# Kernel optimization log

Hardware: AMD Instinct MI355X
Metric: run time of the kernel (lower is better)

The kernel has to match this reference:

```python
import jax, jax.numpy as jnp
import numpy as np

EMBEDDING_DIM = 100
M = 50                      # chunk width
NUM_CHUNK = EMBEDDING_DIM // M  # 2
VOCAB = 100000
EPS = 1e-8                  # torch CosineSimilarity eps


def setup_inputs() -> dict:
    key = jax.random.key(0)
    k_idx, k_emb, k_w, k_u = jax.random.split(key, 4)
    word_idxs = jax.random.randint(k_idx, (4096, 200), 0, VOCAB)  # [B, L]
    # embedding table initialized uniform(-1, 1) as in the original np.random.uniform
    emb_table = jax.random.uniform(k_emb, (VOCAB, EMBEDDING_DIM), dtype=jnp.float32,
                                   minval=-1.0, maxval=1.0)
    weights = jnp.ones((EMBEDDING_DIM, 1), dtype=jnp.float32)      # output projection
    attend_u = jnp.ones((NUM_CHUNK, M), dtype=jnp.float32)         # per-chunk attention query
    return {"word_idxs": word_idxs, "emb_table": emb_table,
            "weights": weights, "attend_u": attend_u}


def reference(word_idxs, emb_table, weights, attend_u):
    B, L = word_idxs.shape
    embeds = emb_table[word_idxs]                       # [B, L, 100]
    ch = embeds.reshape(B, L, NUM_CHUNK, M)             # [B, L, C, M]
    # cosine similarity per word vs per-chunk query (torch eps semantics)
    e_norm = ch / jnp.maximum(jnp.linalg.norm(ch, axis=-1, keepdims=True), EPS)
    u_norm = attend_u / jnp.maximum(jnp.linalg.norm(attend_u, axis=-1, keepdims=True), EPS)
    cos = jnp.einsum('blcm,cm->blc', e_norm, u_norm)    # [B, L, C]
    alphas = jnp.exp(cos)                               # positive -> L1 norm == sum
    norm_alphas = alphas / jnp.sum(alphas, axis=1, keepdims=True)
    hidden = jnp.einsum('blcm,blc->bcm', ch, norm_alphas).reshape(B, EMBEDDING_DIM)
    return hidden @ weights                             # [B, 1]
```

## Files before the change

kernel.cpp:

```cpp
#include <hip/hip_runtime.h>

constexpr int C_ = 2;
constexpr int M_ = 50;
constexpr int ED = 100;
constexpr float EPS = 1e-8f;

constexpr int ROWS = 128;
constexpr int PAD  = 101;

__global__ __launch_bounds__(128) void row_stats_kernel(
    const float* __restrict__ emb,
    const float* __restrict__ wgt,
    const float* __restrict__ att,
    float4*      __restrict__ tbl,
    int vocab)
{
    __shared__ float  s_rows[ROWS * PAD];
    __shared__ float2 s_uw[ED];
    __shared__ float  s_su[C_];

    const int t  = threadIdx.x;
    const int r0 = blockIdx.x * ROWS;

    if (t < ED) s_uw[t] = make_float2(att[t], wgt[t]);
    __syncthreads();
    if (t < C_) {
        float ss = 0.f;
        #pragma unroll
        for (int m = 0; m < M_; ++m) { float v = s_uw[t * M_ + m].x; ss += v * v; }
        s_su[t] = 1.0f / fmaxf(sqrtf(ss), EPS);
    }

    const int nrows = min(ROWS, vocab - r0);
    const int nvec  = nrows * (ED / 4);
    const float4* src = reinterpret_cast<const float4*>(emb + (long long)r0 * ED);
    for (int i = t; i < nvec; i += 128) {
        const float4 v = src[i];
        const int F   = i * 4;
        const int row = F / ED;
        const int col = F - row * ED;
        float* d = &s_rows[row * PAD + col];
        d[0] = v.x; d[1] = v.y; d[2] = v.z; d[3] = v.w;
    }
    __syncthreads();

    if (t < nrows) {
        const float* row = &s_rows[t * PAD];
        float sq0 = 0.f, sq1 = 0.f, du0 = 0.f, du1 = 0.f, dw0 = 0.f, dw1 = 0.f;
        #pragma unroll
        for (int e = 0; e < M_; ++e) {
            const float x = row[e];
            const float2 uw = s_uw[e];
            sq0 += x * x; du0 = fmaf(x, uw.x, du0); dw0 = fmaf(x, uw.y, dw0);
        }
        #pragma unroll
        for (int e = M_; e < ED; ++e) {
            const float x = row[e];
            const float2 uw = s_uw[e];
            sq1 += x * x; du1 = fmaf(x, uw.x, du1); dw1 = fmaf(x, uw.y, dw1);
        }
        const float c0 = du0 / fmaxf(sqrtf(sq0), EPS) * s_su[0];
        const float c1 = du1 / fmaxf(sqrtf(sq1), EPS) * s_su[1];
        const float a0 = __expf(c0);
        const float a1 = __expf(c1);
        tbl[r0 + t] = make_float4(a0, a1, a0 * dw0, a1 * dw1);
    }
}

__global__ __launch_bounds__(256) void attend_kernel(
    const int*    __restrict__ idx,
    const float4* __restrict__ tbl,
    float*        __restrict__ out,
    int B, int L)
{
    const int wave = threadIdx.x >> 6;
    const int lane = threadIdx.x & 63;
    const int b    = blockIdx.x * 4 + wave;
    if (b >= B) return;

    const int* ib = idx + (long long)b * L;
    float a0 = 0.f, a1 = 0.f, ap0 = 0.f, ap1 = 0.f;
    #pragma unroll 4
    for (int l = lane; l < L; l += 64) {
        const float4 v = tbl[ib[l]];
        a0 += v.x; a1 += v.y; ap0 += v.z; ap1 += v.w;
    }

    #pragma unroll
    for (int off = 32; off > 0; off >>= 1) {
        a0  += __shfl_down(a0,  off, 64);
        a1  += __shfl_down(a1,  off, 64);
        ap0 += __shfl_down(ap0, off, 64);
        ap1 += __shfl_down(ap1, off, 64);
    }
    if (lane == 0) out[b] = ap0 / a0 + ap1 / a1;
}

extern "C" void kernel_launch(void* const* d_in, const int* in_sizes, int n_in,
                              void* d_out, int out_size, void* d_ws, size_t ws_size,
                              hipStream_t stream) {
    const int*   idx = (const int*)d_in[0];
    const float* emb = (const float*)d_in[1];
    const float* wgt = (const float*)d_in[2];
    const float* att = (const float*)d_in[3];
    float* out = (float*)d_out;

    const int B     = out_size;
    const int L     = in_sizes[0] / B;
    const int vocab = in_sizes[1] / ED;

    float4* tbl = (float4*)d_ws;

    row_stats_kernel<<<(vocab + ROWS - 1) / ROWS, 128, 0, stream>>>(emb, wgt, att, tbl, vocab);
    attend_kernel<<<(B + 3) / 4, 256, 0, stream>>>(idx, tbl, out, B, L);
}
```

Before: 103.2 us.

## Compute per-row stats with two threads per row reading global directly

Replaces the shared-memory staging of 128-row tiles with a direct global load where each thread handles one 50-wide chunk of a row via float2 loads, pairing the two halves with a lane shuffle before writing the float4 table entry. It removes the large LDS tile and its sync, raising occupancy and doubling thread count. In exchange, global loads are strided by 200 bytes between lanes, so accesses are less coalesced per instruction and rely on cache reuse. A lane that returns early on the bounds check could feed undefined data to its partner's shuffle.

```diff
diff --git a/kernel.cpp b/kernel.cpp
--- a/kernel.cpp
+++ b/kernel.cpp
@@ -5,23 +5,17 @@
 constexpr int ED = 100;
 constexpr float EPS = 1e-8f;
 
-constexpr int ROWS = 128;
-constexpr int PAD  = 101;
-
-__global__ __launch_bounds__(128) void row_stats_kernel(
+__global__ __launch_bounds__(256) void row_stats_kernel(
     const float* __restrict__ emb,
     const float* __restrict__ wgt,
     const float* __restrict__ att,
     float4*      __restrict__ tbl,
     int vocab)
 {
-    __shared__ float  s_rows[ROWS * PAD];
     __shared__ float2 s_uw[ED];
     __shared__ float  s_su[C_];
 
-    const int t  = threadIdx.x;
-    const int r0 = blockIdx.x * ROWS;
-
+    const int t = threadIdx.x;
     if (t < ED) s_uw[t] = make_float2(att[t], wgt[t]);
     __syncthreads();
     if (t < C_) {
@@ -30,41 +24,31 @@
         for (int m = 0; m < M_; ++m) { float v = s_uw[t * M_ + m].x; ss += v * v; }
         s_su[t] = 1.0f / fmaxf(sqrtf(ss), EPS);
     }
-
-    const int nrows = min(ROWS, vocab - r0);
-    const int nvec  = nrows * (ED / 4);
-    const float4* src = reinterpret_cast<const float4*>(emb + (long long)r0 * ED);
-    for (int i = t; i < nvec; i += 128) {
-        const float4 v = src[i];
-        const int F   = i * 4;
-        const int row = F / ED;
-        const int col = F - row * ED;
-        float* d = &s_rows[row * PAD + col];
-        d[0] = v.x; d[1] = v.y; d[2] = v.z; d[3] = v.w;
-    }
     __syncthreads();
 
-    if (t < nrows) {
-        const float* row = &s_rows[t * PAD];
-        float sq0 = 0.f, sq1 = 0.f, du0 = 0.f, du1 = 0.f, dw0 = 0.f, dw1 = 0.f;
-        #pragma unroll
-        for (int e = 0; e < M_; ++e) {
-            const float x = row[e];
-            const float2 uw = s_uw[e];
-            sq0 += x * x; du0 = fmaf(x, uw.x, du0); dw0 = fmaf(x, uw.y, dw0);
-        }
-        #pragma unroll
-        for (int e = M_; e < ED; ++e) {
-            const float x = row[e];
-            const float2 uw = s_uw[e];
-            sq1 += x * x; du1 = fmaf(x, uw.x, du1); dw1 = fmaf(x, uw.y, dw1);
-        }
-        const float c0 = du0 / fmaxf(sqrtf(sq0), EPS) * s_su[0];
-        const float c1 = du1 / fmaxf(sqrtf(sq1), EPS) * s_su[1];
-        const float a0 = __expf(c0);
-        const float a1 = __expf(c1);
-        tbl[r0 + t] = make_float4(a0, a1, a0 * dw0, a1 * dw1);
+    const int h = blockIdx.x * 256 + t;
+    if (h >= 2 * vocab) return;
+    const int r = h >> 1;
+    const int c = h & 1;
+
+    const float2* p = reinterpret_cast<const float2*>(emb + (long long)r * ED + c * M_);
+    float sq = 0.f, du = 0.f, dw = 0.f;
+    #pragma unroll
+    for (int j = 0; j < M_ / 2; ++j) {
+        const float2 v = p[j];
+        const float2 uw0 = s_uw[c * M_ + 2 * j];
+        const float2 uw1 = s_uw[c * M_ + 2 * j + 1];
+        sq  = fmaf(v.x, v.x, sq);  sq = fmaf(v.y, v.y, sq);
+        du  = fmaf(v.x, uw0.x, du); du = fmaf(v.y, uw1.x, du);
+        dw  = fmaf(v.x, uw0.y, dw); dw = fmaf(v.y, uw1.y, dw);
     }
+    const float cosv = du / fmaxf(sqrtf(sq), EPS) * s_su[c];
+    const float a    = __expf(cosv);
+    const float ap   = a * dw;
+
+    const float a_o  = __shfl_xor(a,  1, 64);
+    const float ap_o = __shfl_xor(ap, 1, 64);
+    if (c == 0) tbl[r] = make_float4(a, a_o, ap, ap_o);
 }
 
 __global__ __launch_bounds__(256) void attend_kernel(
@@ -111,6 +95,7 @@
 
     float4* tbl = (float4*)d_ws;
 
-    row_stats_kernel<<<(vocab + ROWS - 1) / ROWS, 128, 0, stream>>>(emb, wgt, att, tbl, vocab);
+    const int halves = 2 * vocab;
+    row_stats_kernel<<<(halves + 255) / 256, 256, 0, stream>>>(emb, wgt, att, tbl, vocab);
     attend_kernel<<<(B + 3) / 4, 256, 0, stream>>>(idx, tbl, out, B, L);
 }
```

Result: faster. 94.71 us (-8.3%).
